# Kernel optimization log

Hardware: AMD Instinct MI355X
Metric: run time of the kernel (lower is better)

Reference implementation:

```python
import jax, jax.numpy as jnp
from jax import lax
import numpy as np

WINDOW = 8
ENCOLEN = 128
HID = 128
INT_H = 128


def setup_inputs() -> dict:
    key = jax.random.key(0)
    ks = jax.random.split(key, 16)
    s = 0.05
    B, T = 512, 256
    return {
        "input_X": jax.random.normal(ks[0], (B, T, 7), jnp.float32),
        "W_ih": jax.random.normal(ks[1], (4 * HID, 5), jnp.float32) * s,
        "W_hh": jax.random.normal(ks[2], (4 * HID, HID), jnp.float32) * s,
        "b_ih": jax.random.normal(ks[3], (4 * HID,), jnp.float32) * s,
        "b_hh": jax.random.normal(ks[4], (4 * HID,), jnp.float32) * s,
        "fc1_w": jax.random.normal(ks[5], (HID, HID), jnp.float32) * s,
        "fc1_b": jax.random.normal(ks[6], (HID,), jnp.float32) * s,
        "fc2_w": jax.random.normal(ks[7], (1, HID), jnp.float32) * s,
        "fc2_b": jax.random.normal(ks[8], (1,), jnp.float32) * s,
        "int1_w": jax.random.normal(ks[9], (INT_H, 3), jnp.float32) * s,
        "int1_b": jax.random.normal(ks[10], (INT_H,), jnp.float32) * s,
        "int3_w": jax.random.normal(ks[11], (1, INT_H), jnp.float32) * s,
        "int3_b": jax.random.normal(ks[12], (1,), jnp.float32) * s,
        "scale_w": jax.random.normal(ks[13], (1, 1), jnp.float32) * s,
        "zone_w": jax.random.normal(ks[14], (1, 1), jnp.float32) * s,
    }


def _forward(input_X, W_ih, W_hh, b_ih, b_hh, fc1_w, fc1_b, fc2_w, fc2_b,
             int1_w, int1_b, int3_w, int3_b, scale_w, zone_w):
    B, T, _ = input_X.shape
    w = WINDOW
    T0 = input_X[:, :, 0:1]      # zone temperature
    Ext_X = input_X[:, :, 1:5]   # cols [1,2,3,4]
    Int_X = input_X[:, :, 3:6]   # cols [3,4,5]
    HVAC_X = input_X[:, :, 6:7]  # col [6]

    def lstm_chunk(h, c, xs):  # xs: [B, w, 5]
        def step(carry, x_t):
            h, c = carry
            g = x_t @ W_ih.T + b_ih + h @ W_hh.T + b_hh
            gi, gf, gg, go = jnp.split(g, 4, axis=-1)  # torch gate order i,f,g,o
            c = jax.nn.sigmoid(gf) * c + jax.nn.sigmoid(gi) * jnp.tanh(gg)
            h = jax.nn.sigmoid(go) * jnp.tanh(c)
            return (h, c), None
        (h, c), _ = lax.scan(step, (h, c), jnp.swapaxes(xs, 0, 1))
        return h, c  # final h == lstm_out[:, -1, :]

    def ext_module(h, c, xs):
        h, c = lstm_chunk(h, c, xs)
        o = jax.nn.relu(h @ fc1_w.T + fc1_b)
        return o @ fc2_w.T + fc2_b, h, c  # [B,1]

    # internal module is pointwise per timestep -> vectorize over all T
    # (note: FC2 in the torch module is defined but unused; faithful skip)
    int_all = jax.nn.sigmoid(
        jax.nn.relu(Int_X @ int1_w.T + int1_b) @ int3_w.T + int3_b
    ) @ scale_w.T  # [B,T,1]

    TOut = jnp.zeros((B, T, 1), input_X.dtype).at[:, :w].set(T0[:, :w])
    h = jnp.ones((B, HID), input_X.dtype)
    c = jnp.ones((B, HID), input_X.dtype)
    E = T0[:, w:w + 1, :]  # [B,1,1]

    def enc_step(carry, i):
        TOut, h, c, E = carry
        ratio = i.astype(input_X.dtype) / ENCOLEN
        TOut = lax.dynamic_update_slice(TOut, E, (0, i, 0))
        s = i - w + 1
        Tin = lax.dynamic_slice(T0, (0, s, 0), (B, w, 1))
        TOsl = lax.dynamic_slice(TOut, (0, s, 0), (B, w, 1))
        Exsl = lax.dynamic_slice(Ext_X, (0, s, 0), (B, w, 4))
        embed = jnp.concatenate([Tin * ratio + TOsl * (1.0 - ratio), Exsl], axis=2)
        ext, h, c = ext_module(h, c, embed)
        hv = lax.dynamic_slice(HVAC_X, (0, i, 0), (B, 1, 1))[:, 0]
        it = lax.dynamic_slice(int_all, (0, i, 0), (B, 1, 1))[:, 0]
        total = ext + hv + it  # [B,1]
        T0i = lax.dynamic_slice(T0, (0, i, 0), (B, 1, 1))
        E = ratio * T0i + (1.0 - ratio) * E + (total @ zone_w.T)[:, None, :]
        return (TOut, h, c, E), ext

    (TOut, h, c, E), ext_enc = lax.scan(enc_step, (TOut, h, c, E), jnp.arange(w, ENCOLEN))

    def dec_step(carry, i):
        TOut, h, c, E = carry
        TOut = lax.dynamic_update_slice(TOut, E, (0, i, 0))
        s = i - w + 1
        TOsl = lax.dynamic_slice(TOut, (0, s, 0), (B, w, 1))
        Exsl = lax.dynamic_slice(Ext_X, (0, s, 0), (B, w, 4))
        embed = jnp.concatenate([TOsl, Exsl], axis=2)
        ext, h, c = ext_module(h, c, embed)
        hv = lax.dynamic_slice(HVAC_X, (0, i, 0), (B, 1, 1))[:, 0]
        it = lax.dynamic_slice(int_all, (0, i, 0), (B, 1, 1))[:, 0]
        total = ext + hv + it
        E = (total @ zone_w.T)[:, None, :] + E
        return (TOut, h, c, E), ext

    (TOut, h, c, E), ext_dec = lax.scan(dec_step, (TOut, h, c, E), jnp.arange(ENCOLEN, T))

    Ext_list = jnp.zeros((B, T, 1), input_X.dtype)
    Ext_list = Ext_list.at[:, w:ENCOLEN].set(jnp.swapaxes(ext_enc, 0, 1))
    Ext_list = Ext_list.at[:, ENCOLEN:].set(jnp.swapaxes(ext_dec, 0, 1))
    Int_list = jnp.zeros((B, T, 1), input_X.dtype).at[:, w:].set(int_all[:, w:])
    HVAC_list = HVAC_X  # torch fills HVAC_list with HVAC_X at every step
    return TOut, HVAC_list, (Ext_list, Int_list)


def reference(input_X, W_ih, W_hh, b_ih, b_hh, fc1_w, fc1_b, fc2_w, fc2_b,
              int1_w, int1_b, int3_w, int3_b, scale_w, zone_w):
    return _forward(input_X, W_ih, W_hh, b_ih, b_hh, fc1_w, fc1_b, fc2_w, fc2_b,
                    int1_w, int1_b, int3_w, int3_b, scale_w, zone_w)
```

## Files before the change

### kernel.cpp

```cpp
#include <hip/hip_runtime.h>

#define BT   (512*256)
#define HB0b 128
#define HB1b 288
#define HLENb 448

using short8  = __attribute__((ext_vector_type(8))) short;
using floatx4 = __attribute__((ext_vector_type(4))) float;
using int4v   = __attribute__((ext_vector_type(4))) int;

__device__ inline unsigned short f2bf(float f){
  unsigned int u = __float_as_uint(f);
  u += 0x7FFFu + ((u >> 16) & 1u);
  return (unsigned short)(u >> 16);
}
__device__ inline float bf2f(unsigned short u){
  return __uint_as_float(((unsigned int)u) << 16);
}
__device__ inline float rcpf(float x){ return __builtin_amdgcn_rcpf(x); }

__global__ __launch_bounds__(512,1) void k_seq(
    const float* __restrict__ in,
    const float* __restrict__ Wih,  const float* __restrict__ Whh,
    const float* __restrict__ bih,  const float* __restrict__ bhh,
    const float* __restrict__ fc1w, const float* __restrict__ fc1b,
    const float* __restrict__ fc2w, const float* __restrict__ fc2b,
    const float* __restrict__ i1w,  const float* __restrict__ i1b,
    const float* __restrict__ i3w,  const float* __restrict__ i3b,
    const float* __restrict__ scw,  const float* __restrict__ zonew,
    float* __restrict__ out)
{
  __shared__ __align__(16) signed char hbuf[2][HLENb];
  __shared__ __align__(16) unsigned short xg[8192];
  __shared__ __align__(8)  unsigned short toutl[512];
  __shared__ __align__(8)  unsigned short extl[512];
  __shared__ __align__(16) unsigned short exl[2048];
  __shared__ float t0l[512];
  __shared__ float hvitl[512];
  __shared__ float parts[16];

  const int tid = threadIdx.x;
  const int wv  = tid >> 6;
  const int ln  = tid & 63;
  const int l15 = ln & 15;
  const int quad= ln >> 4;
  const int bb  = blockIdx.x;

  {
    int b=tid>>8, tt=tid&255;
    const float* row = in + (2*bb+b)*1792 + tt*7;
    t0l[tid] = row[0];
    exl[tid*4+0]=f2bf(row[1]); exl[tid*4+1]=f2bf(row[2]);
    exl[tid*4+2]=f2bf(row[3]); exl[tid*4+3]=f2bf(row[4]);
  }
  for(int p=tid; p<2*HLENb; p+=512) ((signed char*)hbuf)[p]=0;
  if(tid<16) toutl[(tid>>3)*256+(tid&7)] = f2bf(in[(2*bb+(tid>>3))*1792+(tid&7)*7]);
  float* lw4 = (float*)&xg[0];
  float* l3  = lw4 + 512;
  if(tid<128){
    lw4[tid*4+0]=i1w[tid*3+0]; lw4[tid*4+1]=i1w[tid*3+1];
    lw4[tid*4+2]=i1w[tid*3+2]; lw4[tid*4+3]=i1b[tid];
    l3[tid]=i3w[tid];
  }
  __syncthreads();
  if(tid<256) hbuf[0][((tid>>7)? HB1b:HB0b) + (tid&127)] = 127;

  {
    const float b30=i3b[0], sc0=scw[0];
    int b=tid>>8, t=tid&255;
    const float* row = in + (2*bb+b)*1792 + t*7;
    float x0=row[3],x1=row[4],x2=row[5], acc=0.f;
    #pragma unroll 8
    for(int j=0;j<128;j++){
      float r=fmaxf(lw4[j*4]*x0+lw4[j*4+1]*x1+lw4[j*4+2]*x2+lw4[j*4+3],0.f);
      acc += r*l3[j];
    }
    float v = rcpf(1.f+__expf(-(acc+b30)))*sc0;
    float itv = (t<8)?0.f:v;
    int gb = 2*bb+b;
    hvitl[tid] = row[6] + itv;
    out[3*BT+gb*256+t]=itv;
    out[BT+gb*256+t]=row[6];
    if(t<8){ out[gb*256+t]=row[0]; out[2*BT+gb*256+t]=0.f; }
  }

  int4v wq[4][2];
  float dq[4];
  short8 xfr[4];
  float  bsum[4];
  #pragma unroll
  for(int g=0;g<4;g++){
    int n = 128*g + 16*wv + l15;
    bsum[g] = bih[n]+bhh[n];
    const float* wr = Whh + n*128;
    float mx = 1e-20f;
    for(int j=0;j<128;j++) mx = fmaxf(mx, fabsf(wr[j]));
    float qs = 127.f/mx;
    dq[g] = mx * (1.f/16129.f);
    #pragma unroll
    for(int c=0;c<2;c++){
      int4v v4;
      #pragma unroll
      for(int d=0;d<4;d++){
        int pk=0;
        #pragma unroll
        for(int bq=0;bq<4;bq++){
          int kk = c*64 + quad*16 + d*4 + bq;
          int q = __float2int_rn(wr[kk]*qs);
          pk |= (q & 255) << (8*bq);
        }
        v4[d]=pk;
      }
      wq[g][c]=v4;
    }
    short8 f;
    #pragma unroll
    for(int j=0;j<8;j++){ int kk=quad*8+j; f[j]=(short)f2bf(kk<5?Wih[n*5+kk]:0.f); }
    xfr[g]=f;
  }
  int4v fq[2]; float dqf;
  {
    int n2 = 16*wv + l15;
    const float* fr = fc1w + n2*128;
    float mx = 1e-20f;
    for(int j=0;j<128;j++) mx = fmaxf(mx, fabsf(fr[j]));
    float qs = 127.f/mx;
    dqf = mx * (1.f/16129.f);
    #pragma unroll
    for(int c=0;c<2;c++){
      int4v v4;
      #pragma unroll
      for(int d=0;d<4;d++){
        int pk=0;
        #pragma unroll
        for(int bq=0;bq<4;bq++){
          int kk = c*64 + quad*16 + d*4 + bq;
          int q = __float2int_rn(fr[kk]*qs);
          pk |= (q & 255) << (8*bq);
        }
        v4[d]=pk;
      }
      fq[c]=v4;
    }
  }

  const int  u     = 16*wv + l15;
  const int  bm    = quad & 1;
  const int  arow  = ((l15&3)==0) ? (((l15>>2)&1)? HB1b : HB0b) : 0;
  const int  aoff  = arow + quad*16;
  const int  xbase = bm*512 + u;
  const int  hwoff = (bm? HB1b:HB0b) + u;
  const float fb    = fc1b[u];
  const float fcw_u = fc2w[u];
  const float fc2b0 = fc2b[0];
  const float zwv   = zonew[0];
  const floatx4 ZV  = {0.f,0.f,0.f,0.f};
  const int4v   ZI  = {0,0,0,0};
  const short8  Z8  = 0;
  float E0 = in[(2*bb)*1792 + 56];
  float E1 = in[(2*bb+1)*1792 + 56];
  float c0 = 1.f;
  __syncthreads();

  #pragma unroll 1
  for(int i=8;i<256;i++){
    if(i>8){
      float ext0 = parts[0]+parts[2]+parts[4]+parts[6]
                 + parts[8]+parts[10]+parts[12]+parts[14] + fc2b0;
      float ext1 = parts[1]+parts[3]+parts[5]+parts[7]
                 + parts[9]+parts[11]+parts[13]+parts[15] + fc2b0;
      int ip = i-1;
      float tot0 = ext0 + hvitl[ip];
      float tot1 = ext1 + hvitl[256+ip];
      if(ip<128){
        float ratio=(float)ip*0.0078125f;
        E0 = ratio*t0l[ip]     + (1.f-ratio)*E0 + tot0*zwv;
        E1 = ratio*t0l[256+ip] + (1.f-ratio)*E1 + tot1*zwv;
      } else {
        E0 += tot0*zwv;
        E1 += tot1*zwv;
      }
      if(tid==0){ extl[ip]=f2bf(ext0); extl[256+ip]=f2bf(ext1); }
    }
    if(tid==0){ toutl[i]=f2bf(E0); toutl[256+i]=f2bf(E1); }
    {
      short8 ea = Z8;
      if(quad==0){
        int bE=l15>>3, kk=l15&7, p=i-7+kk;
        float tos = (p==i) ? (bE? E1:E0) : bf2f(toutl[bE*256+p]);
        float tmix;
        if(i<128){
          float ratio=(float)i*0.0078125f;
          tmix = t0l[bE*256+p]*ratio + tos*(1.f-ratio);
        } else tmix = tos;
        ea[0]=(short)f2bf(tmix);
        ea[1]=(short)exl[(bE*256+p)*4+0]; ea[2]=(short)exl[(bE*256+p)*4+1];
        ea[3]=(short)exl[(bE*256+p)*4+2]; ea[4]=(short)exl[(bE*256+p)*4+3];
      }
      #pragma unroll
      for(int g=0;g<4;g++){
        floatx4 z=__builtin_amdgcn_mfma_f32_16x16x32_bf16(ea, xfr[g], ZV,0,0,0);
        #pragma unroll
        for(int r=0;r<4;r++){
          int m=4*quad+r;
          xg[(m&7)*1024 + (m>>3)*512 + 128*g + u] = f2bf(z[r]+bsum[g]);
        }
      }
    }
    __syncthreads();

    #pragma unroll
    for(int k=0;k<8;k++){
      float xv0=bf2f(xg[k*1024+xbase    ]);
      float xv1=bf2f(xg[k*1024+xbase+128]);
      float xv2=bf2f(xg[k*1024+xbase+256]);
      float xv3=bf2f(xg[k*1024+xbase+384]);
      const signed char* hb = &hbuf[k&1][0];
      int4v a0 = *(const int4v*)(hb + aoff);
      int4v a1 = *(const int4v*)(hb + aoff + 64);
      int4v acc[4];
      #pragma unroll
      for(int g=0;g<4;g++){
        int4v z = __builtin_amdgcn_mfma_i32_16x16x64_i8(a0, wq[g][0], ZI,0,0,0);
        z = __builtin_amdgcn_mfma_i32_16x16x64_i8(a1, wq[g][1], z,0,0,0);
        acc[g]=z;
      }
      float gi=(float)acc[0][0]*dq[0]+xv0;
      float gf=(float)acc[1][0]*dq[1]+xv1;
      float gg=(float)acc[2][0]*dq[2]+xv2;
      float go=(float)acc[3][0]*dq[3]+xv3;
      float ef =__expf(-gf);
      float egi=__expf(-gi);
      float egg=__expf(-2.f*gg);
      float sf = rcpf(1.f+ef);
      float itn=(1.f-egg)*rcpf((1.f+egi)*(1.f+egg));
      c0 = sf*c0 + itn;
      float ego=__expf(-go);
      float ec =__expf(-2.f*c0);
      float hv2=(1.f-ec)*rcpf((1.f+ego)*(1.f+ec));
      int q = __float2int_rn(hv2*127.f);
      hbuf[(k+1)&1][hwoff] = (signed char)q;
      __syncthreads();
    }

    {
      const signed char* hb = &hbuf[0][0];
      int4v a0 = *(const int4v*)(hb + aoff);
      int4v a1 = *(const int4v*)(hb + aoff + 64);
      int4v z = __builtin_amdgcn_mfma_i32_16x16x64_i8(a0, fq[0], ZI,0,0,0);
      z = __builtin_amdgcn_mfma_i32_16x16x64_i8(a1, fq[1], z,0,0,0);
      float fv = (float)z[0]*dqf + fb;
      float pv = fmaxf(fv,0.f)*fcw_u;
      float v0 = (quad==0) ? pv : 0.f;
      float v1 = (quad==1) ? pv : 0.f;
      #pragma unroll
      for(int off=32; off; off>>=1){
        v0 += __shfl_xor(v0, off, 64);
        v1 += __shfl_xor(v1, off, 64);
      }
      if(ln==0){ parts[wv*2]=v0; parts[wv*2+1]=v1; }
    }
    __syncthreads();
  }

  if(tid==0){
    float ext0 = parts[0]+parts[2]+parts[4]+parts[6]
               + parts[8]+parts[10]+parts[12]+parts[14] + fc2b0;
    float ext1 = parts[1]+parts[3]+parts[5]+parts[7]
               + parts[9]+parts[11]+parts[13]+parts[15] + fc2b0;
    extl[255]=f2bf(ext0); extl[511]=f2bf(ext1);
  }
  __syncthreads();

  for(int p=tid; p<496; p+=512){
    int b = (p>=248) ? 1 : 0;
    int i2 = p - b*248 + 8;
    int gb = 2*bb + b;
    out[gb*256+i2]      = bf2f(toutl[b*256+i2]);
    out[2*BT+gb*256+i2] = bf2f(extl[b*256+i2]);
  }
}

extern "C" void kernel_launch(void* const* d_in, const int* in_sizes, int n_in,
                              void* d_out, int out_size, void* d_ws, size_t ws_size,
                              hipStream_t stream)
{
  const float* in   = (const float*)d_in[0];
  const float* Wih  = (const float*)d_in[1];
  const float* Whh  = (const float*)d_in[2];
  const float* bih  = (const float*)d_in[3];
  const float* bhh  = (const float*)d_in[4];
  const float* fc1w = (const float*)d_in[5];
  const float* fc1b = (const float*)d_in[6];
  const float* fc2w = (const float*)d_in[7];
  const float* fc2b = (const float*)d_in[8];
  const float* i1w  = (const float*)d_in[9];
  const float* i1b  = (const float*)d_in[10];
  const float* i3w  = (const float*)d_in[11];
  const float* i3b  = (const float*)d_in[12];
  const float* scw  = (const float*)d_in[13];
  const float* zw   = (const float*)d_in[14];
  float* out = (float*)d_out;

  k_seq<<<dim3(256), dim3(512), 0, stream>>>(in, Wih, Whh, bih, bhh,
                                             fc1w, fc1b, fc2w, fc2b,
                                             i1w, i1b, i3w, i3b, scw, zw, out);
}
```

Baseline: 1.080 ms.

## Process one batch row per block with 512 blocks and two blocks per CU

Each block now handles a single batch element instead of two, so 512 blocks launch and the launch bound allows two blocks per CU. Shared buffers are halved and the x-gate buffer is re-laid out so each thread reads its four gate values with two 32-bit loads. The two chained int8 MFMAs per gate become independent MFMAs summed afterwards, shortening the dependency chain. The trade-off is that half of each MFMA's M dimension is now wasted and more blocks compete for the CUs, in exchange for more concurrency to hide the latency of the serial recurrence.

New measurement: 2.186 ms. +102.3%, slower.

```diff
diff --git a/kernel.cpp b/kernel.cpp
--- a/kernel.cpp
+++ b/kernel.cpp
@@ -2,8 +2,6 @@
 
 #define BT   (512*256)
 #define HB0b 128
-#define HB1b 288
-#define HLENb 448
 
 using short8  = __attribute__((ext_vector_type(8))) short;
 using floatx4 = __attribute__((ext_vector_type(4))) float;
@@ -19,7 +17,7 @@
 }
 __device__ inline float rcpf(float x){ return __builtin_amdgcn_rcpf(x); }
 
-__global__ __launch_bounds__(512,1) void k_seq(
+__global__ __launch_bounds__(512,2) void k_seq(
     const float* __restrict__ in,
     const float* __restrict__ Wih,  const float* __restrict__ Whh,
     const float* __restrict__ bih,  const float* __restrict__ bhh,
@@ -30,14 +28,14 @@
     const float* __restrict__ scw,  const float* __restrict__ zonew,
     float* __restrict__ out)
 {
-  __shared__ __align__(16) signed char hbuf[2][HLENb];
-  __shared__ __align__(16) unsigned short xg[8192];
-  __shared__ __align__(8)  unsigned short toutl[512];
-  __shared__ __align__(8)  unsigned short extl[512];
-  __shared__ __align__(16) unsigned short exl[2048];
-  __shared__ float t0l[512];
-  __shared__ float hvitl[512];
-  __shared__ float parts[16];
+  __shared__ __align__(16) signed char hbuf[2][256];
+  __shared__ __align__(16) unsigned short xg[4096];
+  __shared__ __align__(8)  unsigned short toutl[256];
+  __shared__ __align__(8)  unsigned short extl[256];
+  __shared__ __align__(16) unsigned short exl[1024];
+  __shared__ float t0l[256];
+  __shared__ float hvitl[256];
+  __shared__ float parts[8];
 
   const int tid = threadIdx.x;
   const int wv  = tid >> 6;
@@ -46,15 +44,14 @@
   const int quad= ln >> 4;
   const int bb  = blockIdx.x;
 
-  {
-    int b=tid>>8, tt=tid&255;
-    const float* row = in + (2*bb+b)*1792 + tt*7;
+  if(tid < 256){
+    const float* row = in + bb*1792 + tid*7;
     t0l[tid] = row[0];
     exl[tid*4+0]=f2bf(row[1]); exl[tid*4+1]=f2bf(row[2]);
     exl[tid*4+2]=f2bf(row[3]); exl[tid*4+3]=f2bf(row[4]);
   }
-  for(int p=tid; p<2*HLENb; p+=512) ((signed char*)hbuf)[p]=0;
-  if(tid<16) toutl[(tid>>3)*256+(tid&7)] = f2bf(in[(2*bb+(tid>>3))*1792+(tid&7)*7]);
+  ((signed char*)hbuf)[tid] = 0;
+  if(tid<8) toutl[tid] = f2bf(in[bb*1792 + tid*7]);
   float* lw4 = (float*)&xg[0];
   float* l3  = lw4 + 512;
   if(tid<128){
@@ -63,12 +60,11 @@
     l3[tid]=i3w[tid];
   }
   __syncthreads();
-  if(tid<256) hbuf[0][((tid>>7)? HB1b:HB0b) + (tid&127)] = 127;
-
-  {
+  if(tid<128) hbuf[0][HB0b + tid] = 127;
+
+  if(tid < 256){
     const float b30=i3b[0], sc0=scw[0];
-    int b=tid>>8, t=tid&255;
-    const float* row = in + (2*bb+b)*1792 + t*7;
+    const float* row = in + bb*1792 + tid*7;
     float x0=row[3],x1=row[4],x2=row[5], acc=0.f;
     #pragma unroll 8
     for(int j=0;j<128;j++){
@@ -76,12 +72,11 @@
       acc += r*l3[j];
     }
     float v = rcpf(1.f+__expf(-(acc+b30)))*sc0;
-    float itv = (t<8)?0.f:v;
-    int gb = 2*bb+b;
+    float itv = (tid<8)?0.f:v;
     hvitl[tid] = row[6] + itv;
-    out[3*BT+gb*256+t]=itv;
-    out[BT+gb*256+t]=row[6];
-    if(t<8){ out[gb*256+t]=row[0]; out[2*BT+gb*256+t]=0.f; }
+    out[3*BT+bb*256+tid]=itv;
+    out[BT+bb*256+tid]=row[6];
+    if(tid<8){ out[bb*256+tid]=row[0]; out[2*BT+bb*256+tid]=0.f; }
   }
 
   int4v wq[4][2];
@@ -145,11 +140,8 @@
   }
 
   const int  u     = 16*wv + l15;
-  const int  bm    = quad & 1;
-  const int  arow  = ((l15&3)==0) ? (((l15>>2)&1)? HB1b : HB0b) : 0;
-  const int  aoff  = arow + quad*16;
-  const int  xbase = bm*512 + u;
-  const int  hwoff = (bm? HB1b:HB0b) + u;
+  const int  aoff  = (((l15&3)==0) ? HB0b : 0) + quad*16;
+  const int  hwoff = HB0b + u;
   const float fb    = fc1b[u];
   const float fcw_u = fc2w[u];
   const float fc2b0 = fc2b[0];
@@ -157,53 +149,49 @@
   const floatx4 ZV  = {0.f,0.f,0.f,0.f};
   const int4v   ZI  = {0,0,0,0};
   const short8  Z8  = 0;
-  float E0 = in[(2*bb)*1792 + 56];
-  float E1 = in[(2*bb+1)*1792 + 56];
+  float E0 = in[bb*1792 + 56];
   float c0 = 1.f;
   __syncthreads();
 
   #pragma unroll 1
   for(int i=8;i<256;i++){
     if(i>8){
-      float ext0 = parts[0]+parts[2]+parts[4]+parts[6]
-                 + parts[8]+parts[10]+parts[12]+parts[14] + fc2b0;
-      float ext1 = parts[1]+parts[3]+parts[5]+parts[7]
-                 + parts[9]+parts[11]+parts[13]+parts[15] + fc2b0;
+      float ext0 = parts[0]+parts[1]+parts[2]+parts[3]
+                 + parts[4]+parts[5]+parts[6]+parts[7] + fc2b0;
       int ip = i-1;
       float tot0 = ext0 + hvitl[ip];
-      float tot1 = ext1 + hvitl[256+ip];
       if(ip<128){
         float ratio=(float)ip*0.0078125f;
-        E0 = ratio*t0l[ip]     + (1.f-ratio)*E0 + tot0*zwv;
-        E1 = ratio*t0l[256+ip] + (1.f-ratio)*E1 + tot1*zwv;
+        E0 = ratio*t0l[ip] + (1.f-ratio)*E0 + tot0*zwv;
       } else {
         E0 += tot0*zwv;
-        E1 += tot1*zwv;
-      }
-      if(tid==0){ extl[ip]=f2bf(ext0); extl[256+ip]=f2bf(ext1); }
-    }
-    if(tid==0){ toutl[i]=f2bf(E0); toutl[256+i]=f2bf(E1); }
+      }
+      if(tid==0) extl[ip]=f2bf(ext0);
+    }
+    if(tid==0) toutl[i]=f2bf(E0);
     {
       short8 ea = Z8;
-      if(quad==0){
-        int bE=l15>>3, kk=l15&7, p=i-7+kk;
-        float tos = (p==i) ? (bE? E1:E0) : bf2f(toutl[bE*256+p]);
+      if(quad==0 && l15<8){
+        int p = i-7+l15;
+        float tos = (l15==7) ? E0 : bf2f(toutl[p]);
         float tmix;
         if(i<128){
           float ratio=(float)i*0.0078125f;
-          tmix = t0l[bE*256+p]*ratio + tos*(1.f-ratio);
+          tmix = t0l[p]*ratio + tos*(1.f-ratio);
         } else tmix = tos;
         ea[0]=(short)f2bf(tmix);
-        ea[1]=(short)exl[(bE*256+p)*4+0]; ea[2]=(short)exl[(bE*256+p)*4+1];
-        ea[3]=(short)exl[(bE*256+p)*4+2]; ea[4]=(short)exl[(bE*256+p)*4+3];
+        ea[1]=(short)exl[p*4+0]; ea[2]=(short)exl[p*4+1];
+        ea[3]=(short)exl[p*4+2]; ea[4]=(short)exl[p*4+3];
       }
       #pragma unroll
       for(int g=0;g<4;g++){
         floatx4 z=__builtin_amdgcn_mfma_f32_16x16x32_bf16(ea, xfr[g], ZV,0,0,0);
-        #pragma unroll
-        for(int r=0;r<4;r++){
-          int m=4*quad+r;
-          xg[(m&7)*1024 + (m>>3)*512 + 128*g + u] = f2bf(z[r]+bsum[g]);
+        if(quad<2){
+          #pragma unroll
+          for(int r=0;r<4;r++){
+            int k=4*quad+r;
+            xg[k*512 + u*4 + g] = f2bf(z[r]+bsum[g]);
+          }
         }
       }
     }
@@ -211,24 +199,25 @@
 
     #pragma unroll
     for(int k=0;k<8;k++){
-      float xv0=bf2f(xg[k*1024+xbase    ]);
-      float xv1=bf2f(xg[k*1024+xbase+128]);
-      float xv2=bf2f(xg[k*1024+xbase+256]);
-      float xv3=bf2f(xg[k*1024+xbase+384]);
+      const unsigned int* xp = (const unsigned int*)&xg[k*512 + u*4];
+      unsigned int xlo = xp[0], xhi = xp[1];
+      float xv0 = __uint_as_float(xlo << 16);
+      float xv1 = __uint_as_float(xlo & 0xffff0000u);
+      float xv2 = __uint_as_float(xhi << 16);
+      float xv3 = __uint_as_float(xhi & 0xffff0000u);
       const signed char* hb = &hbuf[k&1][0];
       int4v a0 = *(const int4v*)(hb + aoff);
       int4v a1 = *(const int4v*)(hb + aoff + 64);
-      int4v acc[4];
+      int4v p0[4], p1[4];
       #pragma unroll
       for(int g=0;g<4;g++){
-        int4v z = __builtin_amdgcn_mfma_i32_16x16x64_i8(a0, wq[g][0], ZI,0,0,0);
-        z = __builtin_amdgcn_mfma_i32_16x16x64_i8(a1, wq[g][1], z,0,0,0);
-        acc[g]=z;
-      }
-      float gi=(float)acc[0][0]*dq[0]+xv0;
-      float gf=(float)acc[1][0]*dq[1]+xv1;
-      float gg=(float)acc[2][0]*dq[2]+xv2;
-      float go=(float)acc[3][0]*dq[3]+xv3;
+        p0[g] = __builtin_amdgcn_mfma_i32_16x16x64_i8(a0, wq[g][0], ZI,0,0,0);
+        p1[g] = __builtin_amdgcn_mfma_i32_16x16x64_i8(a1, wq[g][1], ZI,0,0,0);
+      }
+      float gi=(float)(p0[0][0]+p1[0][0])*dq[0]+xv0;
+      float gf=(float)(p0[1][0]+p1[1][0])*dq[1]+xv1;
+      float gg=(float)(p0[2][0]+p1[2][0])*dq[2]+xv2;
+      float go=(float)(p0[3][0]+p1[3][0])*dq[3]+xv3;
       float ef =__expf(-gf);
       float egi=__expf(-gi);
       float egg=__expf(-2.f*gg);
@@ -238,8 +227,10 @@
       float ego=__expf(-go);
       float ec =__expf(-2.f*c0);
       float hv2=(1.f-ec)*rcpf((1.f+ego)*(1.f+ec));
-      int q = __float2int_rn(hv2*127.f);
-      hbuf[(k+1)&1][hwoff] = (signed char)q;
+      if(quad==0){
+        int q = __float2int_rn(hv2*127.f);
+        hbuf[(k+1)&1][hwoff] = (signed char)q;
+      }
       __syncthreads();
     }
 
@@ -247,37 +238,30 @@
       const signed char* hb = &hbuf[0][0];
       int4v a0 = *(const int4v*)(hb + aoff);
       int4v a1 = *(const int4v*)(hb + aoff + 64);
-      int4v z = __builtin_amdgcn_mfma_i32_16x16x64_i8(a0, fq[0], ZI,0,0,0);
-      z = __builtin_amdgcn_mfma_i32_16x16x64_i8(a1, fq[1], z,0,0,0);
-      float fv = (float)z[0]*dqf + fb;
+      int4v z0 = __builtin_amdgcn_mfma_i32_16x16x64_i8(a0, fq[0], ZI,0,0,0);
+      int4v z1 = __builtin_amdgcn_mfma_i32_16x16x64_i8(a1, fq[1], ZI,0,0,0);
+      float fv = (float)(z0[0]+z1[0])*dqf + fb;
       float pv = fmaxf(fv,0.f)*fcw_u;
       float v0 = (quad==0) ? pv : 0.f;
-      float v1 = (quad==1) ? pv : 0.f;
-      #pragma unroll
-      for(int off=32; off; off>>=1){
-        v0 += __shfl_xor(v0, off, 64);
-        v1 += __shfl_xor(v1, off, 64);
-      }
-      if(ln==0){ parts[wv*2]=v0; parts[wv*2+1]=v1; }
+      #pragma unroll
+      for(int off=32; off; off>>=1) v0 += __shfl_xor(v0, off, 64);
+      if(ln==0) parts[wv]=v0;
     }
     __syncthreads();
   }
 
   if(tid==0){
-    float ext0 = parts[0]+parts[2]+parts[4]+parts[6]
-               + parts[8]+parts[10]+parts[12]+parts[14] + fc2b0;
-    float ext1 = parts[1]+parts[3]+parts[5]+parts[7]
-               + parts[9]+parts[11]+parts[13]+parts[15] + fc2b0;
-    extl[255]=f2bf(ext0); extl[511]=f2bf(ext1);
+    float ext0 = parts[0]+parts[1]+parts[2]+parts[3]
+               + parts[4]+parts[5]+parts[6]+parts[7] + fc2b0;
+    extl[255]=f2bf(ext0);
   }
   __syncthreads();
 
-  for(int p=tid; p<496; p+=512){
-    int b = (p>=248) ? 1 : 0;
-    int i2 = p - b*248 + 8;
-    int gb = 2*bb + b;
-    out[gb*256+i2]      = bf2f(toutl[b*256+i2]);
-    out[2*BT+gb*256+i2] = bf2f(extl[b*256+i2]);
+  if(tid < 496){
+    int isT = (tid < 248);
+    int i2 = (isT ? tid : tid-248) + 8;
+    if(isT) out[bb*256+i2]      = bf2f(toutl[i2]);
+    else    out[2*BT+bb*256+i2] = bf2f(extl[i2]);
   }
 }
 
@@ -302,7 +286,7 @@
   const float* zw   = (const float*)d_in[14];
   float* out = (float*)d_out;
 
-  k_seq<<<dim3(256), dim3(512), 0, stream>>>(in, Wih, Whh, bih, bhh,
+  k_seq<<<dim3(512), dim3(512), 0, stream>>>(in, Wih, Whh, bih, bhh,
                                              fc1w, fc1b, fc2w, fc2b,
                                              i1w, i1b, i3w, i3b, scw, zw, out);
 }
```
